# Performance work log

Hardware: AMD Instinct MI355X
Metric: run time of the kernel (lower is better)

## Reference

```python
import jax, jax.numpy as jnp
import numpy as np

B, C_IN, C_OUT, H, W = 16, 64, 64, 256, 256
M1, M2 = 20, 20


def setup_inputs() -> dict:
    key = jax.random.key(0)
    kx, kr, ki = jax.random.split(key, 3)
    scale = 1.0 / (C_IN * C_OUT)
    x = jax.random.normal(kx, (B, C_IN, H, W), dtype=jnp.float32)
    w_real = scale * jax.random.normal(kr, (C_IN, C_OUT, M1, M2), dtype=jnp.float32)
    w_imag = scale * jax.random.normal(ki, (C_IN, C_OUT, M1, M2), dtype=jnp.float32)
    return {"x": x, "w_real": w_real, "w_imag": w_imag}


def reference(x, w_real, w_imag):
    # x: [B, C_in, H, W] real
    Bn, Cin, Hn, Wn = x.shape
    w = jax.lax.complex(w_real, w_imag)  # [C_in, C_out, M1, M2]
    x_ft = jnp.fft.rfft2(x)              # [B, C_in, H, W//2+1] complex
    # Truncate to the retained low modes (top-left corner only, as in the torch code)
    x_low = x_ft[:, :, :M1, :M2]
    # Complex channel mixing: 'bixy,ioxy->boxy'
    out_low = jnp.einsum('bixy,ioxy->boxy', x_low, w)
    # Zero-pad back to full spectral size
    Wf = x_ft.shape[-1]
    out_ft = jnp.zeros((Bn, w.shape[1], Hn, Wf), dtype=out_low.dtype)
    out_ft = out_ft.at[:, :, :M1, :M2].set(out_low)
    out = jnp.fft.irfft2(out_ft, s=(Hn, Wn))  # [B, C_out, H, W] real
    return out
```

## Files before the change

### kernel.cpp

```cpp
#include <hip/hip_runtime.h>

constexpr int NB = 16;
constexpr int NCI = 64;
constexpr int NCO = 64;
constexpr int NH = 256;
constexpr int NW = 256;
constexpr int NM1 = 20;
constexpr int NM2 = 20;
constexpr int NMODES = 400;

constexpr long OFF_TWS  = 0;
constexpr long OFF_TINV = 12288;
constexpr long OFF_XL   = OFF_TINV + 7680;
constexpr long OFF_OL   = OFF_XL + (long)NB*NCI*NMODES*2;

constexpr float TWO_PI = 6.28318530717958647692f;
constexpr float INV_N2 = 1.0f / 65536.0f;

__device__ __forceinline__ void gload16(const float* g, float* l) {
    __builtin_amdgcn_global_load_lds(
        (const __attribute__((address_space(1))) unsigned int*)(g),
        (__attribute__((address_space(3))) unsigned int*)(l), 16, 0, 0);
}

__global__ void init_tabs(float* __restrict__ ws) {
    int e = blockIdx.x * 256 + threadIdx.x;
    if (e < 12288) {
        int w = e / 48, s = e % 48;
        int cg = s / 12, q = s % 12;
        float v = 0.f;
        if (q < 10) {
            int n = 10 * cg + q, ky = n >> 1, p = n & 1;
            float ang = TWO_PI * (float)((ky * w) & 255) * (1.0f / 256.0f);
            float sn, cn; sincosf(ang, &sn, &cn);
            v = p ? -sn : cn;
        }
        ws[OFF_TWS + e] = v;
    } else if (e < 19968) {
        int f = e - 12288;
        int tb = f / 3840, rr = f % 3840;
        int ky = rr / 192, g = (rr % 192) / 12, q = rr % 12;
        float v = 0.f;
        if (q < 8) {
            int w = 8 * g + 1 + q;
            float ang = TWO_PI * (float)((ky * w) & 255) * (1.0f / 256.0f);
            float sn, cn; sincosf(ang, &sn, &cn);
            float cky = (ky == 0) ? 1.0f : 2.0f;
            v = (tb == 0 ? cn : sn) * cky * INV_N2;
        }
        ws[OFF_TINV + f] = v;
    }
}

__launch_bounds__(256, 2)
__global__ void fwd_kernel(const float* __restrict__ x, float* __restrict__ ws) {
    __shared__ float sm[10752];
    float* sA = sm;
    float2* csp = (float2*)(sm + 10240);
    const int t = threadIdx.x;
    const int r = blockIdx.x;
    const float* xr = x + (long)r * (NH * NW);

    const int wid  = t >> 6;
    const int lane = t & 63;
    const int widu = __builtin_amdgcn_readfirstlane(wid);
    const float* twsu = ws + OFF_TWS + 12 * widu;
    const int keyr = (lane >> 1) & 3;
    const bool swapEO = (wid & 1);

    const int jsrc = (lane & 3) ^ ((lane >> 3) & 3);
    const int srcoff = ((jsrc >> 1) << 2) + ((jsrc & 1) << 7);
    const int srow = lane >> 2;

    float acc[4][10];
#pragma unroll
    for (int a0 = 0; a0 < 4; a0++)
#pragma unroll
        for (int a1 = 0; a1 < 10; a1++) acc[a0][a1] = 0.f;

#define STAGE(KC, BUF)                                                         \
    {                                                                          \
        const float* xs_ = xr + (KC) * 8 + srcoff;                             \
        _Pragma("unroll")                                                      \
        for (int ii = 0; ii < 16; ++ii)                                        \
            gload16(xs_ + (long)(ii * 16 + srow) * NW, (BUF) + ii * 256);      \
    }

    {
        float ang = TWO_PI * (float)t * (1.0f / 256.0f);
        float s, c; sincosf(ang, &s, &c);
        csp[t] = make_float2(c, s);
    }
    STAGE(0, sm);
    __syncthreads();

    for (int kc = 0; kc < 16; ++kc) {
        float* buf = sm + (kc & 1) * 4096;
        if (kc < 15) STAGE(kc + 1, sm + ((kc + 1) & 1) * 4096);
#pragma unroll
        for (int g = 0; g < 2; ++g) {
            float4 f4[4], b4[4];
#pragma unroll
            for (int rr = 0; rr < 4; ++rr) {
                const float* rp = buf + (lane + 64 * rr) * 16;
                f4[rr] = *(const float4*)(rp + 4 * ((2 * g)     ^ keyr));
                b4[rr] = *(const float4*)(rp + 4 * ((2 * g + 1) ^ keyr));
            }
#pragma unroll
            for (int e = 0; e < 4; ++e) {
                const float* tp = twsu + (long)(kc * 8 + 4 * g + e) * 48;
                float4 t0 = *(const float4*)(tp);
                float4 t1 = *(const float4*)(tp + 4);
                float4 t2 = *(const float4*)(tp + 8);
                float tv[10] = {t0.x,t0.y,t0.z,t0.w, t1.x,t1.y,t1.z,t1.w, t2.x,t2.y};
#pragma unroll
                for (int rr = 0; rr < 4; ++rr) {
                    float fv = f4[rr][e], bv = b4[rr][e];
                    float mu = fv + bv, mv = fv - bv;
                    float mE = swapEO ? mv : mu;
                    float mO = swapEO ? mu : mv;
                    acc[rr][0] += mE * tv[0];  acc[rr][1] += mE * tv[1];
                    acc[rr][2] += mO * tv[2];  acc[rr][3] += mO * tv[3];
                    acc[rr][4] += mE * tv[4];  acc[rr][5] += mE * tv[5];
                    acc[rr][6] += mO * tv[6];  acc[rr][7] += mO * tv[7];
                    acc[rr][8] += mE * tv[8];  acc[rr][9] += mE * tv[9];
                }
            }
        }
        __syncthreads();
    }
#undef STAGE

#pragma unroll
    for (int rr = 0; rr < 4; ++rr)
#pragma unroll
        for (int q = 0; q < 10; ++q)
            sA[(lane + 64 * rr) * 40 + 10 * wid + q] = acc[rr][q];
    __syncthreads();

    if (t < 200) {
        const int p  = t >> 1;
        const int sh = t & 1;
        const int kxg = p / 10, kyg = p % 10;
        const int kx0 = 2 * kxg;
        float a2[8];
#pragma unroll
        for (int q = 0; q < 8; q++) a2[q] = 0.f;
        for (int it = 0; it < 128; ++it) {
            int h = 128 * sh + it;
            float4 a = *(const float4*)(sA + h * 40 + 4 * kyg);
            int i0 = (kx0 * h) & 255;
            int i1 = (i0 + h) & 255;
            float2 cs0 = csp[i0];
            float2 cs1 = csp[i1];
            a2[0] += a.x*cs0.x + a.y*cs0.y;  a2[1] += a.y*cs0.x - a.x*cs0.y;
            a2[2] += a.z*cs0.x + a.w*cs0.y;  a2[3] += a.w*cs0.x - a.z*cs0.y;
            a2[4] += a.x*cs1.x + a.y*cs1.y;  a2[5] += a.y*cs1.x - a.x*cs1.y;
            a2[6] += a.z*cs1.x + a.w*cs1.y;  a2[7] += a.w*cs1.x - a.z*cs1.y;
        }
#pragma unroll
        for (int q = 0; q < 8; q++) a2[q] += __shfl_xor(a2[q], 1);
        if (sh == 0) {
            float* xl = ws + OFF_XL + (long)r * (NMODES * 2);
            *(float4*)(xl + 2*(kx0*20 + 2*kyg))       = make_float4(a2[0],a2[1],a2[2],a2[3]);
            *(float4*)(xl + 2*((kx0+1)*20 + 2*kyg))   = make_float4(a2[4],a2[5],a2[6],a2[7]);
        }
    }
}

__launch_bounds__(256, 4)
__global__ void mix_kernel(const float* __restrict__ wre, const float* __restrict__ wim,
                           float* __restrict__ ws) {
    const int t = threadIdx.x;
    const int bo = blockIdx.x;
    const int b = bo >> 6, o = bo & 63;
    if (t >= 200) return;
    const float* XLp = ws + OFF_XL + (long)(b * 64) * 800 + 4 * t;
    const float* wrp = wre + (long)o * NMODES + 2 * t;
    const float* wip = wim + (long)o * NMODES + 2 * t;
    float4 a = make_float4(0.f, 0.f, 0.f, 0.f);
#pragma unroll 4
    for (int i = 0; i < 64; ++i) {
        float4 xv  = *(const float4*)(XLp + (long)i * 800);
        float2 wrv = *(const float2*)(wrp + (long)i * (NCO * NMODES));
        float2 wiv = *(const float2*)(wip + (long)i * (NCO * NMODES));
        a.x += xv.x * wrv.x - xv.y * wiv.x;
        a.y += xv.x * wiv.x + xv.y * wrv.x;
        a.z += xv.z * wrv.y - xv.w * wiv.y;
        a.w += xv.z * wiv.y + xv.w * wrv.y;
    }
    *(float4*)(ws + OFF_OL + (long)bo * 800 + 4 * t) = a;
}

__launch_bounds__(256, 3)
__global__ void inv_kernel(const float* __restrict__ ws, float* __restrict__ out) {
    __shared__ float sm2[11712];
    float* sOL = sm2;
    float* cs  = sm2 + 800;
    float* sYr = sm2 + 1312;
    float* sYi = sm2 + 2672;
    float* sTc = sm2 + 4032;
    float* sTs = sm2 + 7872;
    const int t = threadIdx.x;
    const int blk = blockIdx.x;
    const int bo = blk >> 2;
    const int hq = blk & 3;

    { float ang = TWO_PI * (float)t * (1.0f/256.0f); float s,c; sincosf(ang,&s,&c);
      cs[2*t] = c; cs[2*t+1] = s; }
    {
        const float* OL = ws + OFF_OL + (long)bo * (NMODES * 2);
#pragma unroll
        for (int j = 0; j < 4; ++j) {
            int u = t + 256 * j;
            if (u < 800) sOL[u] = OL[u];
        }
        const float* TI = ws + OFF_TINV;
#pragma unroll
        for (int j = 0; j < 8; ++j) {
            int u = t + 256 * j;
            if (u < 1920) *(float4*)(sTc + 4*u) = *(const float4*)(TI + 4*u);
        }
    }
    __syncthreads();

    {
        int hloc = t >> 2, kyq = t & 3;
        int h = hq * 64 + hloc;
        float a[5][2];
#pragma unroll
        for (int kk = 0; kk < 5; kk++) { a[kk][0] = 0.f; a[kk][1] = 0.f; }
        for (int kx = 0; kx < NM1; ++kx) {
            int idx = (kx * h) & 255;
            float c = cs[2*idx], s = cs[2*idx+1];
#pragma unroll
            for (int kk = 0; kk < 5; ++kk) {
                int ky = kyq * 5 + kk;
                float pr = sOL[2*(kx*NM2 + ky)], pi = sOL[2*(kx*NM2 + ky) + 1];
                a[kk][0] += pr * c - pi * s;
                a[kk][1] += pr * s + pi * c;
            }
        }
#pragma unroll
        for (int kk = 0; kk < 5; ++kk) {
            int ky = kyq * 5 + kk;
            sYr[ky*68 + hloc] = a[kk][0];
            sYi[ky*68 + hloc] = a[kk][1];
        }
    }
    __syncthreads();

    {
        const int lg = t & 15;
        const int hg = t >> 4;
        float U[4][8], V[4][8];
#pragma unroll
        for (int rr = 0; rr < 4; rr++)
#pragma unroll
            for (int c = 0; c < 8; c++) { U[rr][c] = 0.f; V[rr][c] = 0.f; }
        for (int ky = 0; ky < 20; ++ky) {
            float4 yr = *(const float4*)(sYr + ky*68 + 4*hg);
            float4 yi = *(const float4*)(sYi + ky*68 + 4*hg);
            const float* tcp = sTc + ky*192 + lg*12;
            const float* tsp = sTs + ky*192 + lg*12;
            float4 c0 = *(const float4*)(tcp), c1 = *(const float4*)(tcp + 4);
            float4 s0 = *(const float4*)(tsp), s1 = *(const float4*)(tsp + 4);
            float ya[4] = {yr.x, yr.y, yr.z, yr.w};
            float yb[4] = {yi.x, yi.y, yi.z, yi.w};
            float tc[8] = {c0.x,c0.y,c0.z,c0.w, c1.x,c1.y,c1.z,c1.w};
            float ts[8] = {s0.x,s0.y,s0.z,s0.w, s1.x,s1.y,s1.z,s1.w};
#pragma unroll
            for (int rr = 0; rr < 4; ++rr)
#pragma unroll
                for (int c = 0; c < 8; ++c) {
                    U[rr][c] += ya[rr] * tc[c];
                    V[rr][c] += yb[rr] * ts[c];
                }
        }
        float* orow0 = out + (long)bo * (NH*NW) + (long)(hq*64 + 4*hg) * NW;
#pragma unroll
        for (int rr = 0; rr < 4; ++rr) {
            float* orow = orow0 + (long)rr * NW;
            float L[8], F[8];
#pragma unroll
            for (int c = 0; c < 8; ++c) { L[c] = U[rr][c] - V[rr][c]; F[c] = U[rr][c] + V[rr][c]; }
            int wl = 8*lg + 1;
            orow[wl] = L[0];
            *(float2*)(orow + wl + 1) = make_float2(L[1], L[2]);
            *(float4*)(orow + wl + 3) = make_float4(L[3], L[4], L[5], L[6]);
            orow[wl + 7] = L[7];
            *(float4*)(orow + 252 - 8*lg) = make_float4(F[3], F[2], F[1], F[0]);
            *(float4*)(orow + 248 - 8*lg) = make_float4(F[7], F[6], F[5], F[4]);
        }
    }
    if (t < 64) {
        float sum = 0.f;
        for (int ky = 0; ky < 20; ++ky)
            sum += sYr[ky*68 + t] * ((ky == 0) ? 1.0f : 2.0f);
        out[(long)bo * (NH*NW) + (long)(hq*64 + t) * NW] = sum * INV_N2;
    }
}

extern "C" void kernel_launch(void* const* d_in, const int* in_sizes, int n_in,
                              void* d_out, int out_size, void* d_ws, size_t ws_size,
                              hipStream_t stream) {
    const float* x   = (const float*)d_in[0];
    const float* wre = (const float*)d_in[1];
    const float* wim = (const float*)d_in[2];
    float* out = (float*)d_out;
    float* ws  = (float*)d_ws;

    init_tabs<<<dim3(78), dim3(256), 0, stream>>>(ws);
    fwd_kernel<<<dim3(NB * NCI), dim3(256), 0, stream>>>(x, ws);
    mix_kernel<<<dim3(1024), dim3(256), 0, stream>>>(wre, wim, ws);
    inv_kernel<<<dim3(NB * NCO * 4), dim3(256), 0, stream>>>(ws, out);
}
```

Baseline: 263.0 us.

## Split forward DFT over two row halves per plane, sum partials in mix

The forward kernel now launches two blocks per input plane, each handling 128 of the 256 rows with half the shared memory and accumulators. Each half writes a partial low-mode spectrum to a separate workspace region, and the mixing kernel adds the two partials before the complex channel contraction. This doubles the number of forward blocks to raise occupancy and parallelism on the memory-bound DFT pass. In exchange it costs extra workspace, an extra global read per element in the mix kernel, and more per-block overhead.

```diff
diff --git a/kernel.cpp b/kernel.cpp
--- a/kernel.cpp
+++ b/kernel.cpp
@@ -12,7 +12,7 @@
 constexpr long OFF_TWS  = 0;
 constexpr long OFF_TINV = 12288;
 constexpr long OFF_XL   = OFF_TINV + 7680;
-constexpr long OFF_OL   = OFF_XL + (long)NB*NCI*NMODES*2;
+constexpr long OFF_OL   = OFF_XL + 2L*NB*NCI*NMODES*2;
 
 constexpr float TWO_PI = 6.28318530717958647692f;
 constexpr float INV_N2 = 1.0f / 65536.0f;
@@ -54,12 +54,14 @@
 
 __launch_bounds__(256, 2)
 __global__ void fwd_kernel(const float* __restrict__ x, float* __restrict__ ws) {
-    __shared__ float sm[10752];
+    __shared__ float sm[5632];
     float* sA = sm;
-    float2* csp = (float2*)(sm + 10240);
+    float2* csp = (float2*)(sm + 5120);
     const int t = threadIdx.x;
-    const int r = blockIdx.x;
-    const float* xr = x + (long)r * (NH * NW);
+    const int bi = blockIdx.x;
+    const int r = bi >> 1;
+    const int s = bi & 1;
+    const float* xr = x + ((long)r << 16) + (s << 15);
 
     const int wid  = t >> 6;
     const int lane = t & 63;
@@ -72,9 +74,9 @@
     const int srcoff = ((jsrc >> 1) << 2) + ((jsrc & 1) << 7);
     const int srow = lane >> 2;
 
-    float acc[4][10];
-#pragma unroll
-    for (int a0 = 0; a0 < 4; a0++)
+    float acc[2][10];
+#pragma unroll
+    for (int a0 = 0; a0 < 2; a0++)
 #pragma unroll
         for (int a1 = 0; a1 < 10; a1++) acc[a0][a1] = 0.f;
 
@@ -82,26 +84,26 @@
     {                                                                          \
         const float* xs_ = xr + (KC) * 8 + srcoff;                             \
         _Pragma("unroll")                                                      \
-        for (int ii = 0; ii < 16; ++ii)                                        \
+        for (int ii = 0; ii < 8; ++ii)                                         \
             gload16(xs_ + (long)(ii * 16 + srow) * NW, (BUF) + ii * 256);      \
     }
 
     {
         float ang = TWO_PI * (float)t * (1.0f / 256.0f);
-        float s, c; sincosf(ang, &s, &c);
-        csp[t] = make_float2(c, s);
+        float sn, cn; sincosf(ang, &sn, &cn);
+        csp[t] = make_float2(cn, sn);
     }
     STAGE(0, sm);
     __syncthreads();
 
     for (int kc = 0; kc < 16; ++kc) {
-        float* buf = sm + (kc & 1) * 4096;
-        if (kc < 15) STAGE(kc + 1, sm + ((kc + 1) & 1) * 4096);
+        float* buf = sm + (kc & 1) * 2048;
+        if (kc < 15) STAGE(kc + 1, sm + ((kc + 1) & 1) * 2048);
 #pragma unroll
         for (int g = 0; g < 2; ++g) {
-            float4 f4[4], b4[4];
-#pragma unroll
-            for (int rr = 0; rr < 4; ++rr) {
+            float4 f4[2], b4[2];
+#pragma unroll
+            for (int rr = 0; rr < 2; ++rr) {
                 const float* rp = buf + (lane + 64 * rr) * 16;
                 f4[rr] = *(const float4*)(rp + 4 * ((2 * g)     ^ keyr));
                 b4[rr] = *(const float4*)(rp + 4 * ((2 * g + 1) ^ keyr));
@@ -114,7 +116,7 @@
                 float4 t2 = *(const float4*)(tp + 8);
                 float tv[10] = {t0.x,t0.y,t0.z,t0.w, t1.x,t1.y,t1.z,t1.w, t2.x,t2.y};
 #pragma unroll
-                for (int rr = 0; rr < 4; ++rr) {
+                for (int rr = 0; rr < 2; ++rr) {
                     float fv = f4[rr][e], bv = b4[rr][e];
                     float mu = fv + bv, mv = fv - bv;
                     float mE = swapEO ? mv : mu;
@@ -132,7 +134,7 @@
 #undef STAGE
 
 #pragma unroll
-    for (int rr = 0; rr < 4; ++rr)
+    for (int rr = 0; rr < 2; ++rr)
 #pragma unroll
         for (int q = 0; q < 10; ++q)
             sA[(lane + 64 * rr) * 40 + 10 * wid + q] = acc[rr][q];
@@ -146,11 +148,12 @@
         float a2[8];
 #pragma unroll
         for (int q = 0; q < 8; q++) a2[q] = 0.f;
-        for (int it = 0; it < 128; ++it) {
-            int h = 128 * sh + it;
-            float4 a = *(const float4*)(sA + h * 40 + 4 * kyg);
-            int i0 = (kx0 * h) & 255;
-            int i1 = (i0 + h) & 255;
+        for (int it = 0; it < 64; ++it) {
+            int hl = 64 * sh + it;
+            int hg = 128 * s + hl;
+            float4 a = *(const float4*)(sA + hl * 40 + 4 * kyg);
+            int i0 = (kx0 * hg) & 255;
+            int i1 = (i0 + hg) & 255;
             float2 cs0 = csp[i0];
             float2 cs1 = csp[i1];
             a2[0] += a.x*cs0.x + a.y*cs0.y;  a2[1] += a.y*cs0.x - a.x*cs0.y;
@@ -161,7 +164,7 @@
 #pragma unroll
         for (int q = 0; q < 8; q++) a2[q] += __shfl_xor(a2[q], 1);
         if (sh == 0) {
-            float* xl = ws + OFF_XL + (long)r * (NMODES * 2);
+            float* xl = ws + OFF_XL + ((long)s * (NB * NCI) + r) * (NMODES * 2);
             *(float4*)(xl + 2*(kx0*20 + 2*kyg))       = make_float4(a2[0],a2[1],a2[2],a2[3]);
             *(float4*)(xl + 2*((kx0+1)*20 + 2*kyg))   = make_float4(a2[4],a2[5],a2[6],a2[7]);
         }
@@ -175,19 +178,23 @@
     const int bo = blockIdx.x;
     const int b = bo >> 6, o = bo & 63;
     if (t >= 200) return;
-    const float* XLp = ws + OFF_XL + (long)(b * 64) * 800 + 4 * t;
+    const float* XL0 = ws + OFF_XL + (long)(b * 64) * 800 + 4 * t;
+    const float* XL1 = XL0 + (long)(NB * NCI) * 800;
     const float* wrp = wre + (long)o * NMODES + 2 * t;
     const float* wip = wim + (long)o * NMODES + 2 * t;
     float4 a = make_float4(0.f, 0.f, 0.f, 0.f);
 #pragma unroll 4
     for (int i = 0; i < 64; ++i) {
-        float4 xv  = *(const float4*)(XLp + (long)i * 800);
+        float4 x0 = *(const float4*)(XL0 + (long)i * 800);
+        float4 x1 = *(const float4*)(XL1 + (long)i * 800);
         float2 wrv = *(const float2*)(wrp + (long)i * (NCO * NMODES));
         float2 wiv = *(const float2*)(wip + (long)i * (NCO * NMODES));
-        a.x += xv.x * wrv.x - xv.y * wiv.x;
-        a.y += xv.x * wiv.x + xv.y * wrv.x;
-        a.z += xv.z * wrv.y - xv.w * wiv.y;
-        a.w += xv.z * wiv.y + xv.w * wrv.y;
+        float xr0 = x0.x + x1.x, xi0 = x0.y + x1.y;
+        float xr1 = x0.z + x1.z, xi1 = x0.w + x1.w;
+        a.x += xr0 * wrv.x - xi0 * wiv.x;
+        a.y += xr0 * wiv.x + xi0 * wrv.x;
+        a.z += xr1 * wrv.y - xi1 * wiv.y;
+        a.w += xr1 * wiv.y + xi1 * wrv.y;
     }
     *(float4*)(ws + OFF_OL + (long)bo * 800 + 4 * t) = a;
 }
@@ -311,7 +318,7 @@
     float* ws  = (float*)d_ws;
 
     init_tabs<<<dim3(78), dim3(256), 0, stream>>>(ws);
-    fwd_kernel<<<dim3(NB * NCI), dim3(256), 0, stream>>>(x, ws);
+    fwd_kernel<<<dim3(2 * NB * NCI), dim3(256), 0, stream>>>(x, ws);
     mix_kernel<<<dim3(1024), dim3(256), 0, stream>>>(wre, wim, ws);
     inv_kernel<<<dim3(NB * NCO * 4), dim3(256), 0, stream>>>(ws, out);
 }
```

New measurement: 268.6 us. 1.02x slower.

## Replace LDS-staged row DFT with per-thread row loads and compact twiddle tables

Applied to the files above, without the earlier changes.

The forward row DFT drops the async global-to-LDS double-buffered staging and wave-split partial-mode scheme. Each thread now reads its own 256-float row directly and accumulates all 40 real/imag outputs using a compact 40-wide twiddle table. The inverse twiddle table is compacted from 12-float to 8-float padded groups, which shrinks LDS use and the number of table loads. The new forward path reads global memory with a per-thread row stride, so its coalescing is poorer, and it needs 40 accumulators per thread, which raises register pressure.

```diff
diff --git a/kernel.cpp b/kernel.cpp
--- a/kernel.cpp
+++ b/kernel.cpp
@@ -17,125 +17,66 @@
 constexpr float TWO_PI = 6.28318530717958647692f;
 constexpr float INV_N2 = 1.0f / 65536.0f;
 
-__device__ __forceinline__ void gload16(const float* g, float* l) {
-    __builtin_amdgcn_global_load_lds(
-        (const __attribute__((address_space(1))) unsigned int*)(g),
-        (__attribute__((address_space(3))) unsigned int*)(l), 16, 0, 0);
-}
-
 __global__ void init_tabs(float* __restrict__ ws) {
     int e = blockIdx.x * 256 + threadIdx.x;
-    if (e < 12288) {
-        int w = e / 48, s = e % 48;
-        int cg = s / 12, q = s % 12;
-        float v = 0.f;
-        if (q < 10) {
-            int n = 10 * cg + q, ky = n >> 1, p = n & 1;
-            float ang = TWO_PI * (float)((ky * w) & 255) * (1.0f / 256.0f);
-            float sn, cn; sincosf(ang, &sn, &cn);
-            v = p ? -sn : cn;
-        }
-        ws[OFF_TWS + e] = v;
-    } else if (e < 19968) {
+    if (e < 5120) {
+        int w = e / 40, n = e % 40;
+        int ky = n >> 1, p = n & 1;
+        float ang = TWO_PI * (float)((ky * w) & 255) * (1.0f / 256.0f);
+        float sn, cn; sincosf(ang, &sn, &cn);
+        ws[OFF_TWS + e] = p ? -sn : cn;
+    } else if (e >= 12288 && e < 17408) {
         int f = e - 12288;
-        int tb = f / 3840, rr = f % 3840;
-        int ky = rr / 192, g = (rr % 192) / 12, q = rr % 12;
-        float v = 0.f;
-        if (q < 8) {
-            int w = 8 * g + 1 + q;
-            float ang = TWO_PI * (float)((ky * w) & 255) * (1.0f / 256.0f);
-            float sn, cn; sincosf(ang, &sn, &cn);
-            float cky = (ky == 0) ? 1.0f : 2.0f;
-            v = (tb == 0 ? cn : sn) * cky * INV_N2;
-        }
-        ws[OFF_TINV + f] = v;
+        int tb = f / 2560, rr2 = f % 2560;
+        int ky = rr2 / 128, g = (rr2 % 128) / 8, q = rr2 % 8;
+        int w = 8 * g + 1 + q;
+        float ang = TWO_PI * (float)((ky * w) & 255) * (1.0f / 256.0f);
+        float sn, cn; sincosf(ang, &sn, &cn);
+        float cky = (ky == 0) ? 1.0f : 2.0f;
+        ws[OFF_TINV + f] = (tb == 0 ? cn : sn) * cky * INV_N2;
     }
 }
 
 __launch_bounds__(256, 2)
 __global__ void fwd_kernel(const float* __restrict__ x, float* __restrict__ ws) {
-    __shared__ float sm[10752];
+    __shared__ float sm[11776];
     float* sA = sm;
-    float2* csp = (float2*)(sm + 10240);
+    float2* csp = (float2*)(sm + 11264);
     const int t = threadIdx.x;
     const int r = blockIdx.x;
-    const float* xr = x + (long)r * (NH * NW);
-
-    const int wid  = t >> 6;
-    const int lane = t & 63;
-    const int widu = __builtin_amdgcn_readfirstlane(wid);
-    const float* twsu = ws + OFF_TWS + 12 * widu;
-    const int keyr = (lane >> 1) & 3;
-    const bool swapEO = (wid & 1);
-
-    const int jsrc = (lane & 3) ^ ((lane >> 3) & 3);
-    const int srcoff = ((jsrc >> 1) << 2) + ((jsrc & 1) << 7);
-    const int srow = lane >> 2;
-
-    float acc[4][10];
-#pragma unroll
-    for (int a0 = 0; a0 < 4; a0++)
-#pragma unroll
-        for (int a1 = 0; a1 < 10; a1++) acc[a0][a1] = 0.f;
-
-#define STAGE(KC, BUF)                                                         \
-    {                                                                          \
-        const float* xs_ = xr + (KC) * 8 + srcoff;                             \
-        _Pragma("unroll")                                                      \
-        for (int ii = 0; ii < 16; ++ii)                                        \
-            gload16(xs_ + (long)(ii * 16 + srow) * NW, (BUF) + ii * 256);      \
-    }
+    const float* row = x + ((long)r << 16) + ((long)t << 8);
+    const float* T = ws + OFF_TWS;
 
     {
         float ang = TWO_PI * (float)t * (1.0f / 256.0f);
-        float s, c; sincosf(ang, &s, &c);
-        csp[t] = make_float2(c, s);
-    }
-    STAGE(0, sm);
-    __syncthreads();
-
-    for (int kc = 0; kc < 16; ++kc) {
-        float* buf = sm + (kc & 1) * 4096;
-        if (kc < 15) STAGE(kc + 1, sm + ((kc + 1) & 1) * 4096);
-#pragma unroll
-        for (int g = 0; g < 2; ++g) {
-            float4 f4[4], b4[4];
-#pragma unroll
-            for (int rr = 0; rr < 4; ++rr) {
-                const float* rp = buf + (lane + 64 * rr) * 16;
-                f4[rr] = *(const float4*)(rp + 4 * ((2 * g)     ^ keyr));
-                b4[rr] = *(const float4*)(rp + 4 * ((2 * g + 1) ^ keyr));
-            }
-#pragma unroll
-            for (int e = 0; e < 4; ++e) {
-                const float* tp = twsu + (long)(kc * 8 + 4 * g + e) * 48;
-                float4 t0 = *(const float4*)(tp);
-                float4 t1 = *(const float4*)(tp + 4);
-                float4 t2 = *(const float4*)(tp + 8);
-                float tv[10] = {t0.x,t0.y,t0.z,t0.w, t1.x,t1.y,t1.z,t1.w, t2.x,t2.y};
-#pragma unroll
-                for (int rr = 0; rr < 4; ++rr) {
-                    float fv = f4[rr][e], bv = b4[rr][e];
-                    float mu = fv + bv, mv = fv - bv;
-                    float mE = swapEO ? mv : mu;
-                    float mO = swapEO ? mu : mv;
-                    acc[rr][0] += mE * tv[0];  acc[rr][1] += mE * tv[1];
-                    acc[rr][2] += mO * tv[2];  acc[rr][3] += mO * tv[3];
-                    acc[rr][4] += mE * tv[4];  acc[rr][5] += mE * tv[5];
-                    acc[rr][6] += mO * tv[6];  acc[rr][7] += mO * tv[7];
-                    acc[rr][8] += mE * tv[8];  acc[rr][9] += mE * tv[9];
-                }
-            }
-        }
-        __syncthreads();
-    }
-#undef STAGE
-
-#pragma unroll
-    for (int rr = 0; rr < 4; ++rr)
-#pragma unroll
-        for (int q = 0; q < 10; ++q)
-            sA[(lane + 64 * rr) * 40 + 10 * wid + q] = acc[rr][q];
+        float sn, cn; sincosf(ang, &sn, &cn);
+        csp[t] = make_float2(cn, sn);
+    }
+
+    float acc[40];
+#pragma unroll
+    for (int n = 0; n < 40; ++n) acc[n] = 0.f;
+
+#pragma unroll 2
+    for (int w4 = 0; w4 < 32; ++w4) {
+        float4 f = *(const float4*)(row + 4 * w4);
+        float4 b = *(const float4*)(row + 128 + 4 * w4);
+#pragma unroll
+        for (int e = 0; e < 4; ++e) {
+            const int w = 4 * w4 + e;
+            const float mu = f[e] + b[e];
+            const float mv = f[e] - b[e];
+            const float* Tw = T + 40 * w;
+#pragma unroll
+            for (int n = 0; n < 40; ++n)
+                acc[n] += (((n >> 1) & 1) ? mv : mu) * Tw[n];
+        }
+    }
+
+#pragma unroll
+    for (int n4 = 0; n4 < 10; ++n4)
+        *(float4*)(sA + t * 44 + 4 * n4) =
+            make_float4(acc[4*n4], acc[4*n4+1], acc[4*n4+2], acc[4*n4+3]);
     __syncthreads();
 
     if (t < 200) {
@@ -148,7 +89,7 @@
         for (int q = 0; q < 8; q++) a2[q] = 0.f;
         for (int it = 0; it < 128; ++it) {
             int h = 128 * sh + it;
-            float4 a = *(const float4*)(sA + h * 40 + 4 * kyg);
+            float4 a = *(const float4*)(sA + h * 44 + 4 * kyg);
             int i0 = (kx0 * h) & 255;
             int i1 = (i0 + h) & 255;
             float2 cs0 = csp[i0];
@@ -194,13 +135,13 @@
 
 __launch_bounds__(256, 3)
 __global__ void inv_kernel(const float* __restrict__ ws, float* __restrict__ out) {
-    __shared__ float sm2[11712];
+    __shared__ float sm2[9152];
     float* sOL = sm2;
     float* cs  = sm2 + 800;
     float* sYr = sm2 + 1312;
     float* sYi = sm2 + 2672;
     float* sTc = sm2 + 4032;
-    float* sTs = sm2 + 7872;
+    float* sTs = sm2 + 6592;
     const int t = threadIdx.x;
     const int blk = blockIdx.x;
     const int bo = blk >> 2;
@@ -217,9 +158,9 @@
         }
         const float* TI = ws + OFF_TINV;
 #pragma unroll
-        for (int j = 0; j < 8; ++j) {
+        for (int j = 0; j < 5; ++j) {
             int u = t + 256 * j;
-            if (u < 1920) *(float4*)(sTc + 4*u) = *(const float4*)(TI + 4*u);
+            if (u < 1280) *(float4*)(sTc + 4*u) = *(const float4*)(TI + 4*u);
         }
     }
     __syncthreads();
@@ -261,8 +202,8 @@
         for (int ky = 0; ky < 20; ++ky) {
             float4 yr = *(const float4*)(sYr + ky*68 + 4*hg);
             float4 yi = *(const float4*)(sYi + ky*68 + 4*hg);
-            const float* tcp = sTc + ky*192 + lg*12;
-            const float* tsp = sTs + ky*192 + lg*12;
+            const float* tcp = sTc + ky*128 + lg*8;
+            const float* tsp = sTs + ky*128 + lg*8;
             float4 c0 = *(const float4*)(tcp), c1 = *(const float4*)(tcp + 4);
             float4 s0 = *(const float4*)(tsp), s1 = *(const float4*)(tsp + 4);
             float ya[4] = {yr.x, yr.y, yr.z, yr.w};
@@ -310,7 +251,7 @@
     float* out = (float*)d_out;
     float* ws  = (float*)d_ws;
 
-    init_tabs<<<dim3(78), dim3(256), 0, stream>>>(ws);
+    init_tabs<<<dim3(68), dim3(256), 0, stream>>>(ws);
     fwd_kernel<<<dim3(NB * NCI), dim3(256), 0, stream>>>(x, ws);
     mix_kernel<<<dim3(1024), dim3(256), 0, stream>>>(wre, wim, ws);
     inv_kernel<<<dim3(NB * NCO * 4), dim3(256), 0, stream>>>(ws, out);
```

Result: no change. 259.1 us, median of 2 (-1.5%).
